# Kernel tuning notes

Hardware: AMD Instinct MI355X
Metric: run time of the kernel (lower is better)

The kernel has to match this reference:

```python
import jax, jax.numpy as jnp
import numpy as np

NEG_INF = -1.0e9


def setup_inputs() -> dict:
    key = jax.random.key(0)
    ks = jax.random.split(key, 8)
    B, H, S, D = 8, 8, 1024, 64
    return {
        "gv_feat": jax.random.normal(ks[0], (B, D), dtype=jnp.float32),
        "query2": jax.random.normal(ks[1], (B, H, S, D), dtype=jnp.float32),
        "key": jax.random.normal(ks[2], (B, H, S, D), dtype=jnp.float32),
        "att_mask": jax.random.randint(ks[3], (B, S), 0, 2, dtype=jnp.int32),
        "value1": jax.random.normal(ks[4], (B, H, S, D), dtype=jnp.float32),
        "value2": jax.random.normal(ks[5], (B, H, S, D), dtype=jnp.float32),
        "W_ch": jax.random.normal(ks[6], (D, D), dtype=jnp.float32) * (1.0 / np.sqrt(D)),
        "b_ch": jnp.zeros((D,), dtype=jnp.float32),
    }


def reference(gv_feat, query2, key, att_mask, value1, value2, W_ch, b_ch):
    # query2/key/value1/value2: [B, H, S, D]; att_mask: [B, S]
    D = query2.shape[-1]
    scaling = D ** (-0.5)
    # spatial attention: masked scaled QK^T softmax
    scores = jnp.einsum("bhqd,bhkd->bhqk", query2, key) * scaling  # [B,H,S,S]
    mask = att_mask[:, None, None, :]  # [B,1,1,S]
    scores = jnp.where(mask == 0, NEG_INF, scores)
    alpha_spatial = jax.nn.softmax(scores, axis=-1)
    attn2 = jnp.einsum("bhqk,bhkd->bhqd", alpha_spatial, value2)  # [B,H,S,D]
    # channel attention: sigmoid-gated linear over elementwise value1*key
    att_map_channel = value1 * key  # [B,H,S,D]
    alpha_channel = jax.nn.sigmoid(
        jnp.einsum("bhsd,ed->bhse", att_map_channel, W_ch) + b_ch
    )
    attn2 = alpha_channel * attn2
    return (gv_feat, attn2)
```

## Files before the change

### kernel.cpp

```cpp
#include <hip/hip_runtime.h>
#include <hip/hip_bf16.h>

typedef __attribute__((ext_vector_type(4)))  float f32x4;
typedef __attribute__((ext_vector_type(16))) float f32x16;
typedef __attribute__((ext_vector_type(8)))  short bf16x8;
typedef __attribute__((ext_vector_type(4)))  unsigned u32x4;
typedef __attribute__((ext_vector_type(2)))  unsigned u32x2;

#define NEG_INF_F (-1000000000.0f)

__device__ inline unsigned pkbf(float a, float b) {
    union { __hip_bfloat16 h; unsigned short u; } x, y;
    x.h = __float2bfloat16(a);
    y.h = __float2bfloat16(b);
    return (unsigned)x.u | ((unsigned)y.u << 16);
}

__global__ __launch_bounds__(1024) void aoa_prep_kernel(
    const int* __restrict__ maskp,
    int* __restrict__ vidx, float* __restrict__ padmask, int* __restrict__ nvalid)
{
    const int b   = blockIdx.x;
    const int tid = threadIdx.x;
    const int lane = tid & 63;

    const int m = maskp[b * 1024 + tid] ? 1 : 0;
    unsigned long long bal = __ballot(m);
    const int wpre = __popcll(bal & ((1ull << lane) - 1ull));

    __shared__ int wsum[16], woff[16];
    if (lane == 63) wsum[tid >> 6] = wpre + m;
    __syncthreads();
    if (tid < 16) {
        int off = 0;
        for (int i = 0; i < tid; ++i) off += wsum[i];
        woff[tid] = off;
    }
    __syncthreads();
    const int pos = woff[tid >> 6] + wpre;
    const int nv  = woff[15] + wsum[15];

    if (m) vidx[b * 1024 + pos] = tid;
    if (tid >= nv) vidx[b * 1024 + tid] = 0;
    padmask[b * 1024 + tid] = (tid < nv) ? 0.0f : NEG_INF_F;
    if (tid == 0) nvalid[b] = nv;
}

__global__ __launch_bounds__(512) void aoa_attn_kernel(
    const float* __restrict__ gv,
    const float* __restrict__ q2,
    const float* __restrict__ keyp,
    const float* __restrict__ v1,
    const float* __restrict__ v2,
    const float* __restrict__ W,
    const float* __restrict__ bch,
    const int*   __restrict__ vidx,
    const float* __restrict__ padmask,
    const int*   __restrict__ nvalid,
    float* __restrict__ out)
{
    constexpr int S = 1024, D = 64;
    const int bh  = blockIdx.x;
    const int qt  = blockIdx.y;
    const int b   = bh >> 3;
    const int tid = threadIdx.x;
    const int wid = tid >> 6;
    const int lane = tid & 63;
    const int l31 = lane & 31;
    const int h   = lane >> 5;

    float* out_attn = out + 512;
    if (bh == 0 && qt == 0) out[tid] = gv[tid];

    __shared__ float pmL[S];
    __shared__ int   vidxL[S];
    __shared__ short Klds[2][64][72];
    __shared__ short Vt[2][64][72];
    __shared__ float Lw[8][32];

    for (int i = tid; i < S; i += 512) {
        pmL[i]   = padmask[b * S + i];
        vidxL[i] = vidx[b * S + i];
    }

    const int nv = nvalid[b];
    const int NT = (nv + 63) >> 6;

    const size_t base = (size_t)bh * S * D;
    const float* Qp  = q2   + base;
    const float* Kp  = keyp + base;
    const float* V1p = v1   + base;
    const float* V2p = v2   + base;

    const int q0   = qt * 256 + wid * 32;
    const int qrow = q0 + l31;

    bf16x8 bq[4];
    #pragma unroll
    for (int ds = 0; ds < 4; ++ds) {
        const f32x4* p = (const f32x4*)(Qp + (size_t)qrow * D + ds * 16 + h * 8);
        f32x4 x0 = p[0], x1 = p[1];
        u32x4 u = (u32x4){pkbf(x0[0], x0[1]), pkbf(x0[2], x0[3]),
                          pkbf(x1[0], x1[1]), pkbf(x1[2], x1[3])};
        bq[ds] = *(bf16x8*)&u;
    }

    f32x16 acc_g[2];
    #pragma unroll
    for (int eh = 0; eh < 2; ++eh)
        #pragma unroll
        for (int r = 0; r < 16; ++r) acc_g[eh][r] = 0.0f;
    {
        bf16x8 bam[4];
        #pragma unroll
        for (int ds = 0; ds < 4; ++ds) {
            const f32x4* p1 = (const f32x4*)(V1p + (size_t)qrow * D + ds * 16 + h * 8);
            const f32x4* pk = (const f32x4*)(Kp  + (size_t)qrow * D + ds * 16 + h * 8);
            f32x4 a0 = p1[0], a1 = p1[1], c0 = pk[0], c1 = pk[1];
            u32x4 u = (u32x4){pkbf(a0[0]*c0[0], a0[1]*c0[1]), pkbf(a0[2]*c0[2], a0[3]*c0[3]),
                              pkbf(a1[0]*c1[0], a1[1]*c1[1]), pkbf(a1[2]*c1[2], a1[3]*c1[3])};
            bam[ds] = *(bf16x8*)&u;
        }
        #pragma unroll
        for (int eh = 0; eh < 2; ++eh) {
            #pragma unroll
            for (int ds = 0; ds < 4; ++ds) {
                const f32x4* pw = (const f32x4*)(W + (size_t)(eh * 32 + l31) * D + ds * 16 + h * 8);
                f32x4 x0 = pw[0], x1 = pw[1];
                u32x4 u = (u32x4){pkbf(x0[0], x0[1]), pkbf(x0[2], x0[3]),
                                  pkbf(x1[0], x1[1]), pkbf(x1[2], x1[3])};
                bf16x8 bw = *(bf16x8*)&u;
                acc_g[eh] = __builtin_amdgcn_mfma_f32_32x32x16_bf16(bam[ds], bw, acc_g[eh], 0, 0, 0);
            }
        }
    }

    f32x16 acc_o[2];
    #pragma unroll
    for (int dh = 0; dh < 2; ++dh)
        #pragma unroll
        for (int r = 0; r < 16; ++r) acc_o[dh][r] = 0.0f;

    float l_run = 0.0f;
    const float SC  = 0.125f * 1.4426950408889634f;
    const float SHF = 12.0f;

    const int kk   = tid >> 3;
    const int d0   = (tid & 7) << 3;
    const int dcol = tid & 63;
    const int kr0  = (tid >> 6) << 3;

    __syncthreads();

    f32x4 kA, kB;
    float vv[8];
    {
        const f32x4* src = (const f32x4*)(Kp + (size_t)vidxL[kk] * D + d0);
        kA = src[0]; kB = src[1];
        #pragma unroll
        for (int i = 0; i < 8; ++i) vv[i] = V2p[(size_t)vidxL[kr0 + i] * D + dcol];
    }
    *(u32x4*)&Klds[0][kk][d0] = (u32x4){pkbf(kA[0], kA[1]), pkbf(kA[2], kA[3]),
                                        pkbf(kB[0], kB[1]), pkbf(kB[2], kB[3])};
    *(u32x4*)&Vt[0][dcol][kr0] = (u32x4){pkbf(vv[0], vv[1]), pkbf(vv[2], vv[3]),
                                         pkbf(vv[4], vv[5]), pkbf(vv[6], vv[7])};
    int cur = 0;

    for (int t = 0; t < NT; ++t) {
        const int kt = t * 64;
        __syncthreads();

        if (t < NT - 1) {
            const f32x4* src = (const f32x4*)(Kp + (size_t)vidxL[kt + 64 + kk] * D + d0);
            kA = src[0]; kB = src[1];
            #pragma unroll
            for (int i = 0; i < 8; ++i) vv[i] = V2p[(size_t)vidxL[kt + 64 + kr0 + i] * D + dcol];
        }

        f32x16 a0;
        #pragma unroll
        for (int r = 0; r < 16; ++r) a0[r] = 0.0f;
        #pragma unroll
        for (int ds = 0; ds < 4; ++ds) {
            bf16x8 ak = *(const bf16x8*)&Klds[cur][l31][ds * 16 + h * 8];
            a0 = __builtin_amdgcn_mfma_f32_32x32x16_bf16(ak, bq[ds], a0, 0, 0, 0);
        }
        f32x16 a1;
        #pragma unroll
        for (int r = 0; r < 16; ++r) a1[r] = 0.0f;
        #pragma unroll
        for (int ds = 0; ds < 4; ++ds) {
            bf16x8 ak = *(const bf16x8*)&Klds[cur][32 + l31][ds * 16 + h * 8];
            a1 = __builtin_amdgcn_mfma_f32_32x32x16_bf16(ak, bq[ds], a1, 0, 0, 0);
        }

        unsigned w0[8];
        {
            float ps0 = 0.f, ps1 = 0.f;
            #pragma unroll
            for (int g = 0; g < 4; ++g) {
                f32x4 mk = *(const f32x4*)&pmL[kt + g * 8 + h * 4];
                float p0 = __builtin_amdgcn_exp2f(fmaf(a0[g * 4 + 0], SC, mk[0]) - SHF);
                float p1 = __builtin_amdgcn_exp2f(fmaf(a0[g * 4 + 1], SC, mk[1]) - SHF);
                float p2 = __builtin_amdgcn_exp2f(fmaf(a0[g * 4 + 2], SC, mk[2]) - SHF);
                float p3 = __builtin_amdgcn_exp2f(fmaf(a0[g * 4 + 3], SC, mk[3]) - SHF);
                ps0 += p0 + p1; ps1 += p2 + p3;
                w0[g * 2]     = pkbf(p0, p1);
                w0[g * 2 + 1] = pkbf(p2, p3);
            }
            float psum = ps0 + ps1;
            psum += __shfl_xor(psum, 32);
            l_run += psum;
        }

        #pragma unroll
        for (int t2 = 0; t2 < 2; ++t2) {
            u32x2 r0 = __builtin_amdgcn_permlane32_swap(w0[t2 * 4 + 0], w0[t2 * 4 + 2], false, false);
            u32x2 r1 = __builtin_amdgcn_permlane32_swap(w0[t2 * 4 + 1], w0[t2 * 4 + 3], false, false);
            u32x4 ua = (u32x4){r0[0], r1[0], r0[1], r1[1]};
            bf16x8 pa = *(bf16x8*)&ua;
            #pragma unroll
            for (int dh = 0; dh < 2; ++dh) {
                bf16x8 bv = *(const bf16x8*)&Vt[cur][dh * 32 + l31][t2 * 16 + h * 8];
                acc_o[dh] = __builtin_amdgcn_mfma_f32_32x32x16_bf16(pa, bv, acc_o[dh], 0, 0, 0);
            }
        }

        unsigned w1[8];
        {
            float ps0 = 0.f, ps1 = 0.f;
            #pragma unroll
            for (int g = 0; g < 4; ++g) {
                f32x4 mk = *(const f32x4*)&pmL[kt + 32 + g * 8 + h * 4];
                float p0 = __builtin_amdgcn_exp2f(fmaf(a1[g * 4 + 0], SC, mk[0]) - SHF);
                float p1 = __builtin_amdgcn_exp2f(fmaf(a1[g * 4 + 1], SC, mk[1]) - SHF);
                float p2 = __builtin_amdgcn_exp2f(fmaf(a1[g * 4 + 2], SC, mk[2]) - SHF);
                float p3 = __builtin_amdgcn_exp2f(fmaf(a1[g * 4 + 3], SC, mk[3]) - SHF);
                ps0 += p0 + p1; ps1 += p2 + p3;
                w1[g * 2]     = pkbf(p0, p1);
                w1[g * 2 + 1] = pkbf(p2, p3);
            }
            float psum = ps0 + ps1;
            psum += __shfl_xor(psum, 32);
            l_run += psum;
        }

        #pragma unroll
        for (int t2 = 0; t2 < 2; ++t2) {
            u32x2 r0 = __builtin_amdgcn_permlane32_swap(w1[t2 * 4 + 0], w1[t2 * 4 + 2], false, false);
            u32x2 r1 = __builtin_amdgcn_permlane32_swap(w1[t2 * 4 + 1], w1[t2 * 4 + 3], false, false);
            u32x4 ua = (u32x4){r0[0], r1[0], r0[1], r1[1]};
            bf16x8 pa = *(bf16x8*)&ua;
            #pragma unroll
            for (int dh = 0; dh < 2; ++dh) {
                bf16x8 bv = *(const bf16x8*)&Vt[cur][dh * 32 + l31][32 + t2 * 16 + h * 8];
                acc_o[dh] = __builtin_amdgcn_mfma_f32_32x32x16_bf16(pa, bv, acc_o[dh], 0, 0, 0);
            }
        }

        if (t < NT - 1) {
            *(u32x4*)&Klds[cur ^ 1][kk][d0] = (u32x4){pkbf(kA[0], kA[1]), pkbf(kA[2], kA[3]),
                                                      pkbf(kB[0], kB[1]), pkbf(kB[2], kB[3])};
            *(u32x4*)&Vt[cur ^ 1][dcol][kr0] = (u32x4){pkbf(vv[0], vv[1]), pkbf(vv[2], vv[3]),
                                                       pkbf(vv[4], vv[5]), pkbf(vv[6], vv[7])};
        }
        cur ^= 1;
    }

    Lw[wid][l31] = 1.0f / l_run;
    __builtin_amdgcn_wave_barrier();
    const float bv0 = bch[l31], bv1 = bch[32 + l31];
    #pragma unroll
    for (int dh = 0; dh < 2; ++dh) {
        const float bc = dh ? bv1 : bv0;
        #pragma unroll
        for (int r = 0; r < 16; ++r) {
            const int ql = (r & 3) + 8 * (r >> 2) + 4 * h;
            float invl = Lw[wid][ql];
            float o = acc_o[dh][r] * invl;
            float z = acc_g[dh][r] + bc;
            float gate = 1.0f / (1.0f + __expf(-z));
            out_attn[base + (size_t)(q0 + ql) * D + dh * 32 + l31] = o * gate;
        }
    }
}

extern "C" void kernel_launch(void* const* d_in, const int* in_sizes, int n_in,
                              void* d_out, int out_size, void* d_ws, size_t ws_size,
                              hipStream_t stream) {
    const float* gv   = (const float*)d_in[0];
    const float* q2   = (const float*)d_in[1];
    const float* keyp = (const float*)d_in[2];
    const int*   mask = (const int*)  d_in[3];
    const float* v1   = (const float*)d_in[4];
    const float* v2   = (const float*)d_in[5];
    const float* W    = (const float*)d_in[6];
    const float* bch  = (const float*)d_in[7];
    float* out = (float*)d_out;

    int*   vidx    = (int*)d_ws;
    float* padmask = (float*)(vidx + 8 * 1024);
    int*   nvalid  = (int*)(padmask + 8 * 1024);

    aoa_prep_kernel<<<8, 1024, 0, stream>>>(mask, vidx, padmask, nvalid);

    dim3 grid(64, 4);
    aoa_attn_kernel<<<grid, 512, 0, stream>>>(gv, q2, keyp, v1, v2, W, bch,
                                              vidx, padmask, nvalid, out);
}
```

Before: 41.24 us.

## Process two query sub-tiles per wave with 256-thread blocks and deferred gate GEMM

Each wave now handles 64 query rows (two 32-row sub-tiles) instead of 32, so every K/V fragment read from LDS feeds twice as many MFMAs. The block shrinks from 512 to 256 threads, and each thread gathers 16 elements per tile instead of 8. The channel-gate GEMM moves after the attention loop to keep register pressure down, and the row-sum reciprocal is broadcast with shuffles instead of going through LDS. The trade-off is twice the accumulator registers per wave and half as many waves per block to hide latency.

```diff
diff --git a/kernel.cpp b/kernel.cpp
--- a/kernel.cpp
+++ b/kernel.cpp
@@ -46,7 +46,7 @@
     if (tid == 0) nvalid[b] = nv;
 }
 
-__global__ __launch_bounds__(512) void aoa_attn_kernel(
+__global__ __launch_bounds__(256, 1) void aoa_attn_kernel(
     const float* __restrict__ gv,
     const float* __restrict__ q2,
     const float* __restrict__ keyp,
@@ -70,15 +70,14 @@
     const int h   = lane >> 5;
 
     float* out_attn = out + 512;
-    if (bh == 0 && qt == 0) out[tid] = gv[tid];
+    if (bh == 0 && qt == 0) { out[tid] = gv[tid]; out[tid + 256] = gv[tid + 256]; }
 
     __shared__ float pmL[S];
     __shared__ int   vidxL[S];
     __shared__ short Klds[2][64][72];
     __shared__ short Vt[2][64][72];
-    __shared__ float Lw[8][32];
-
-    for (int i = tid; i < S; i += 512) {
+
+    for (int i = tid; i < S; i += 256) {
         pmL[i]   = padmask[b * S + i];
         vidxL[i] = vidx[b * S + i];
     }
@@ -92,78 +91,58 @@
     const float* V1p = v1   + base;
     const float* V2p = v2   + base;
 
-    const int q0   = qt * 256 + wid * 32;
-    const int qrow = q0 + l31;
-
-    bf16x8 bq[4];
+    const int q0  = qt * 256 + wid * 64;
+    const int qa  = q0 + l31;
+    const int qb  = q0 + 32 + l31;
+
+    bf16x8 bqa[4], bqb[4];
     #pragma unroll
     for (int ds = 0; ds < 4; ++ds) {
-        const f32x4* p = (const f32x4*)(Qp + (size_t)qrow * D + ds * 16 + h * 8);
-        f32x4 x0 = p[0], x1 = p[1];
-        u32x4 u = (u32x4){pkbf(x0[0], x0[1]), pkbf(x0[2], x0[3]),
-                          pkbf(x1[0], x1[1]), pkbf(x1[2], x1[3])};
-        bq[ds] = *(bf16x8*)&u;
-    }
-
-    f32x16 acc_g[2];
-    #pragma unroll
-    for (int eh = 0; eh < 2; ++eh)
-        #pragma unroll
-        for (int r = 0; r < 16; ++r) acc_g[eh][r] = 0.0f;
-    {
-        bf16x8 bam[4];
-        #pragma unroll
-        for (int ds = 0; ds < 4; ++ds) {
-            const f32x4* p1 = (const f32x4*)(V1p + (size_t)qrow * D + ds * 16 + h * 8);
-            const f32x4* pk = (const f32x4*)(Kp  + (size_t)qrow * D + ds * 16 + h * 8);
-            f32x4 a0 = p1[0], a1 = p1[1], c0 = pk[0], c1 = pk[1];
-            u32x4 u = (u32x4){pkbf(a0[0]*c0[0], a0[1]*c0[1]), pkbf(a0[2]*c0[2], a0[3]*c0[3]),
-                              pkbf(a1[0]*c1[0], a1[1]*c1[1]), pkbf(a1[2]*c1[2], a1[3]*c1[3])};
-            bam[ds] = *(bf16x8*)&u;
-        }
-        #pragma unroll
-        for (int eh = 0; eh < 2; ++eh) {
-            #pragma unroll
-            for (int ds = 0; ds < 4; ++ds) {
-                const f32x4* pw = (const f32x4*)(W + (size_t)(eh * 32 + l31) * D + ds * 16 + h * 8);
-                f32x4 x0 = pw[0], x1 = pw[1];
-                u32x4 u = (u32x4){pkbf(x0[0], x0[1]), pkbf(x0[2], x0[3]),
-                                  pkbf(x1[0], x1[1]), pkbf(x1[2], x1[3])};
-                bf16x8 bw = *(bf16x8*)&u;
-                acc_g[eh] = __builtin_amdgcn_mfma_f32_32x32x16_bf16(bam[ds], bw, acc_g[eh], 0, 0, 0);
-            }
-        }
-    }
-
-    f32x16 acc_o[2];
+        const f32x4* pa = (const f32x4*)(Qp + (size_t)qa * D + ds * 16 + h * 8);
+        f32x4 x0 = pa[0], x1 = pa[1];
+        u32x4 ua = (u32x4){pkbf(x0[0], x0[1]), pkbf(x0[2], x0[3]),
+                           pkbf(x1[0], x1[1]), pkbf(x1[2], x1[3])};
+        bqa[ds] = *(bf16x8*)&ua;
+        const f32x4* pb = (const f32x4*)(Qp + (size_t)qb * D + ds * 16 + h * 8);
+        f32x4 y0 = pb[0], y1 = pb[1];
+        u32x4 ub = (u32x4){pkbf(y0[0], y0[1]), pkbf(y0[2], y0[3]),
+                           pkbf(y1[0], y1[1]), pkbf(y1[2], y1[3])};
+        bqb[ds] = *(bf16x8*)&ub;
+    }
+
+    f32x16 acc_oa[2], acc_ob[2];
     #pragma unroll
     for (int dh = 0; dh < 2; ++dh)
         #pragma unroll
-        for (int r = 0; r < 16; ++r) acc_o[dh][r] = 0.0f;
-
-    float l_run = 0.0f;
+        for (int r = 0; r < 16; ++r) { acc_oa[dh][r] = 0.0f; acc_ob[dh][r] = 0.0f; }
+
+    float l_a = 0.0f, l_b = 0.0f;
     const float SC  = 0.125f * 1.4426950408889634f;
     const float SHF = 12.0f;
 
-    const int kk   = tid >> 3;
-    const int d0   = (tid & 7) << 3;
+    const int kk   = tid >> 2;
+    const int d0   = (tid & 3) << 4;
     const int dcol = tid & 63;
-    const int kr0  = (tid >> 6) << 3;
+    const int kr0  = (tid >> 6) << 4;
 
     __syncthreads();
 
-    f32x4 kA, kB;
-    float vv[8];
+    f32x4 kA0, kA1, kA2, kA3;
+    float vv[16];
     {
         const f32x4* src = (const f32x4*)(Kp + (size_t)vidxL[kk] * D + d0);
-        kA = src[0]; kB = src[1];
-        #pragma unroll
-        for (int i = 0; i < 8; ++i) vv[i] = V2p[(size_t)vidxL[kr0 + i] * D + dcol];
-    }
-    *(u32x4*)&Klds[0][kk][d0] = (u32x4){pkbf(kA[0], kA[1]), pkbf(kA[2], kA[3]),
-                                        pkbf(kB[0], kB[1]), pkbf(kB[2], kB[3])};
-    *(u32x4*)&Vt[0][dcol][kr0] = (u32x4){pkbf(vv[0], vv[1]), pkbf(vv[2], vv[3]),
-                                         pkbf(vv[4], vv[5]), pkbf(vv[6], vv[7])};
+        kA0 = src[0]; kA1 = src[1]; kA2 = src[2]; kA3 = src[3];
+        #pragma unroll
+        for (int i = 0; i < 16; ++i) vv[i] = V2p[(size_t)vidxL[kr0 + i] * D + dcol];
+    }
+    *(u32x4*)&Klds[0][kk][d0]     = (u32x4){pkbf(kA0[0], kA0[1]), pkbf(kA0[2], kA0[3]),
+                                            pkbf(kA1[0], kA1[1]), pkbf(kA1[2], kA1[3])};
+    *(u32x4*)&Klds[0][kk][d0 + 8] = (u32x4){pkbf(kA2[0], kA2[1]), pkbf(kA2[2], kA2[3]),
+                                            pkbf(kA3[0], kA3[1]), pkbf(kA3[2], kA3[3])};
+    *(u32x4*)&Vt[0][dcol][kr0]     = (u32x4){pkbf(vv[0], vv[1]),  pkbf(vv[2], vv[3]),
+                                             pkbf(vv[4], vv[5]),  pkbf(vv[6], vv[7])};
+    *(u32x4*)&Vt[0][dcol][kr0 + 8] = (u32x4){pkbf(vv[8], vv[9]),  pkbf(vv[10], vv[11]),
+                                             pkbf(vv[12], vv[13]), pkbf(vv[14], vv[15])};
     int cur = 0;
 
     for (int t = 0; t < NT; ++t) {
@@ -172,103 +151,192 @@
 
         if (t < NT - 1) {
             const f32x4* src = (const f32x4*)(Kp + (size_t)vidxL[kt + 64 + kk] * D + d0);
-            kA = src[0]; kB = src[1];
-            #pragma unroll
-            for (int i = 0; i < 8; ++i) vv[i] = V2p[(size_t)vidxL[kt + 64 + kr0 + i] * D + dcol];
-        }
-
-        f32x16 a0;
-        #pragma unroll
-        for (int r = 0; r < 16; ++r) a0[r] = 0.0f;
+            kA0 = src[0]; kA1 = src[1]; kA2 = src[2]; kA3 = src[3];
+            #pragma unroll
+            for (int i = 0; i < 16; ++i) vv[i] = V2p[(size_t)vidxL[kt + 64 + kr0 + i] * D + dcol];
+        }
+
+        f32x16 a0a, a1a, a0b, a1b;
+        #pragma unroll
+        for (int r = 0; r < 16; ++r) { a0a[r] = 0.f; a1a[r] = 0.f; a0b[r] = 0.f; a1b[r] = 0.f; }
         #pragma unroll
         for (int ds = 0; ds < 4; ++ds) {
             bf16x8 ak = *(const bf16x8*)&Klds[cur][l31][ds * 16 + h * 8];
-            a0 = __builtin_amdgcn_mfma_f32_32x32x16_bf16(ak, bq[ds], a0, 0, 0, 0);
-        }
-        f32x16 a1;
-        #pragma unroll
-        for (int r = 0; r < 16; ++r) a1[r] = 0.0f;
+            a0a = __builtin_amdgcn_mfma_f32_32x32x16_bf16(ak, bqa[ds], a0a, 0, 0, 0);
+            a0b = __builtin_amdgcn_mfma_f32_32x32x16_bf16(ak, bqb[ds], a0b, 0, 0, 0);
+        }
         #pragma unroll
         for (int ds = 0; ds < 4; ++ds) {
             bf16x8 ak = *(const bf16x8*)&Klds[cur][32 + l31][ds * 16 + h * 8];
-            a1 = __builtin_amdgcn_mfma_f32_32x32x16_bf16(ak, bq[ds], a1, 0, 0, 0);
-        }
-
-        unsigned w0[8];
+            a1a = __builtin_amdgcn_mfma_f32_32x32x16_bf16(ak, bqa[ds], a1a, 0, 0, 0);
+            a1b = __builtin_amdgcn_mfma_f32_32x32x16_bf16(ak, bqb[ds], a1b, 0, 0, 0);
+        }
+
+        unsigned w0a[8], w1a[8], w0b[8], w1b[8];
         {
             float ps0 = 0.f, ps1 = 0.f;
             #pragma unroll
             for (int g = 0; g < 4; ++g) {
                 f32x4 mk = *(const f32x4*)&pmL[kt + g * 8 + h * 4];
-                float p0 = __builtin_amdgcn_exp2f(fmaf(a0[g * 4 + 0], SC, mk[0]) - SHF);
-                float p1 = __builtin_amdgcn_exp2f(fmaf(a0[g * 4 + 1], SC, mk[1]) - SHF);
-                float p2 = __builtin_amdgcn_exp2f(fmaf(a0[g * 4 + 2], SC, mk[2]) - SHF);
-                float p3 = __builtin_amdgcn_exp2f(fmaf(a0[g * 4 + 3], SC, mk[3]) - SHF);
+                float p0 = __builtin_amdgcn_exp2f(fmaf(a0a[g * 4 + 0], SC, mk[0]) - SHF);
+                float p1 = __builtin_amdgcn_exp2f(fmaf(a0a[g * 4 + 1], SC, mk[1]) - SHF);
+                float p2 = __builtin_amdgcn_exp2f(fmaf(a0a[g * 4 + 2], SC, mk[2]) - SHF);
+                float p3 = __builtin_amdgcn_exp2f(fmaf(a0a[g * 4 + 3], SC, mk[3]) - SHF);
                 ps0 += p0 + p1; ps1 += p2 + p3;
-                w0[g * 2]     = pkbf(p0, p1);
-                w0[g * 2 + 1] = pkbf(p2, p3);
+                w0a[g * 2] = pkbf(p0, p1); w0a[g * 2 + 1] = pkbf(p2, p3);
             }
             float psum = ps0 + ps1;
             psum += __shfl_xor(psum, 32);
-            l_run += psum;
-        }
-
+            l_a += psum;
+        }
         #pragma unroll
         for (int t2 = 0; t2 < 2; ++t2) {
-            u32x2 r0 = __builtin_amdgcn_permlane32_swap(w0[t2 * 4 + 0], w0[t2 * 4 + 2], false, false);
-            u32x2 r1 = __builtin_amdgcn_permlane32_swap(w0[t2 * 4 + 1], w0[t2 * 4 + 3], false, false);
+            u32x2 r0 = __builtin_amdgcn_permlane32_swap(w0a[t2 * 4 + 0], w0a[t2 * 4 + 2], false, false);
+            u32x2 r1 = __builtin_amdgcn_permlane32_swap(w0a[t2 * 4 + 1], w0a[t2 * 4 + 3], false, false);
             u32x4 ua = (u32x4){r0[0], r1[0], r0[1], r1[1]};
             bf16x8 pa = *(bf16x8*)&ua;
             #pragma unroll
             for (int dh = 0; dh < 2; ++dh) {
                 bf16x8 bv = *(const bf16x8*)&Vt[cur][dh * 32 + l31][t2 * 16 + h * 8];
-                acc_o[dh] = __builtin_amdgcn_mfma_f32_32x32x16_bf16(pa, bv, acc_o[dh], 0, 0, 0);
-            }
-        }
-
-        unsigned w1[8];
+                acc_oa[dh] = __builtin_amdgcn_mfma_f32_32x32x16_bf16(pa, bv, acc_oa[dh], 0, 0, 0);
+            }
+        }
         {
             float ps0 = 0.f, ps1 = 0.f;
             #pragma unroll
             for (int g = 0; g < 4; ++g) {
-                f32x4 mk = *(const f32x4*)&pmL[kt + 32 + g * 8 + h * 4];
-                float p0 = __builtin_amdgcn_exp2f(fmaf(a1[g * 4 + 0], SC, mk[0]) - SHF);
-                float p1 = __builtin_amdgcn_exp2f(fmaf(a1[g * 4 + 1], SC, mk[1]) - SHF);
-                float p2 = __builtin_amdgcn_exp2f(fmaf(a1[g * 4 + 2], SC, mk[2]) - SHF);
-                float p3 = __builtin_amdgcn_exp2f(fmaf(a1[g * 4 + 3], SC, mk[3]) - SHF);
+                f32x4 mk = *(const f32x4*)&pmL[kt + g * 8 + h * 4];
+                float p0 = __builtin_amdgcn_exp2f(fmaf(a0b[g * 4 + 0], SC, mk[0]) - SHF);
+                float p1 = __builtin_amdgcn_exp2f(fmaf(a0b[g * 4 + 1], SC, mk[1]) - SHF);
+                float p2 = __builtin_amdgcn_exp2f(fmaf(a0b[g * 4 + 2], SC, mk[2]) - SHF);
+                float p3 = __builtin_amdgcn_exp2f(fmaf(a0b[g * 4 + 3], SC, mk[3]) - SHF);
                 ps0 += p0 + p1; ps1 += p2 + p3;
-                w1[g * 2]     = pkbf(p0, p1);
-                w1[g * 2 + 1] = pkbf(p2, p3);
+                w0b[g * 2] = pkbf(p0, p1); w0b[g * 2 + 1] = pkbf(p2, p3);
             }
             float psum = ps0 + ps1;
             psum += __shfl_xor(psum, 32);
-            l_run += psum;
-        }
-
+            l_b += psum;
+        }
         #pragma unroll
         for (int t2 = 0; t2 < 2; ++t2) {
-            u32x2 r0 = __builtin_amdgcn_permlane32_swap(w1[t2 * 4 + 0], w1[t2 * 4 + 2], false, false);
-            u32x2 r1 = __builtin_amdgcn_permlane32_swap(w1[t2 * 4 + 1], w1[t2 * 4 + 3], false, false);
+            u32x2 r0 = __builtin_amdgcn_permlane32_swap(w0b[t2 * 4 + 0], w0b[t2 * 4 + 2], false, false);
+            u32x2 r1 = __builtin_amdgcn_permlane32_swap(w0b[t2 * 4 + 1], w0b[t2 * 4 + 3], false, false);
             u32x4 ua = (u32x4){r0[0], r1[0], r0[1], r1[1]};
             bf16x8 pa = *(bf16x8*)&ua;
             #pragma unroll
             for (int dh = 0; dh < 2; ++dh) {
+                bf16x8 bv = *(const bf16x8*)&Vt[cur][dh * 32 + l31][t2 * 16 + h * 8];
+                acc_ob[dh] = __builtin_amdgcn_mfma_f32_32x32x16_bf16(pa, bv, acc_ob[dh], 0, 0, 0);
+            }
+        }
+        {
+            float ps0 = 0.f, ps1 = 0.f;
+            #pragma unroll
+            for (int g = 0; g < 4; ++g) {
+                f32x4 mk = *(const f32x4*)&pmL[kt + 32 + g * 8 + h * 4];
+                float p0 = __builtin_amdgcn_exp2f(fmaf(a1a[g * 4 + 0], SC, mk[0]) - SHF);
+                float p1 = __builtin_amdgcn_exp2f(fmaf(a1a[g * 4 + 1], SC, mk[1]) - SHF);
+                float p2 = __builtin_amdgcn_exp2f(fmaf(a1a[g * 4 + 2], SC, mk[2]) - SHF);
+                float p3 = __builtin_amdgcn_exp2f(fmaf(a1a[g * 4 + 3], SC, mk[3]) - SHF);
+                ps0 += p0 + p1; ps1 += p2 + p3;
+                w1a[g * 2] = pkbf(p0, p1); w1a[g * 2 + 1] = pkbf(p2, p3);
+            }
+            float psum = ps0 + ps1;
+            psum += __shfl_xor(psum, 32);
+            l_a += psum;
+        }
+        #pragma unroll
+        for (int t2 = 0; t2 < 2; ++t2) {
+            u32x2 r0 = __builtin_amdgcn_permlane32_swap(w1a[t2 * 4 + 0], w1a[t2 * 4 + 2], false, false);
+            u32x2 r1 = __builtin_amdgcn_permlane32_swap(w1a[t2 * 4 + 1], w1a[t2 * 4 + 3], false, false);
+            u32x4 ua = (u32x4){r0[0], r1[0], r0[1], r1[1]};
+            bf16x8 pa = *(bf16x8*)&ua;
+            #pragma unroll
+            for (int dh = 0; dh < 2; ++dh) {
                 bf16x8 bv = *(const bf16x8*)&Vt[cur][dh * 32 + l31][32 + t2 * 16 + h * 8];
-                acc_o[dh] = __builtin_amdgcn_mfma_f32_32x32x16_bf16(pa, bv, acc_o[dh], 0, 0, 0);
+                acc_oa[dh] = __builtin_amdgcn_mfma_f32_32x32x16_bf16(pa, bv, acc_oa[dh], 0, 0, 0);
+            }
+        }
+        {
+            float ps0 = 0.f, ps1 = 0.f;
+            #pragma unroll
+            for (int g = 0; g < 4; ++g) {
+                f32x4 mk = *(const f32x4*)&pmL[kt + 32 + g * 8 + h * 4];
+                float p0 = __builtin_amdgcn_exp2f(fmaf(a1b[g * 4 + 0], SC, mk[0]) - SHF);
+                float p1 = __builtin_amdgcn_exp2f(fmaf(a1b[g * 4 + 1], SC, mk[1]) - SHF);
+                float p2 = __builtin_amdgcn_exp2f(fmaf(a1b[g * 4 + 2], SC, mk[2]) - SHF);
+                float p3 = __builtin_amdgcn_exp2f(fmaf(a1b[g * 4 + 3], SC, mk[3]) - SHF);
+                ps0 += p0 + p1; ps1 += p2 + p3;
+                w1b[g * 2] = pkbf(p0, p1); w1b[g * 2 + 1] = pkbf(p2, p3);
+            }
+            float psum = ps0 + ps1;
+            psum += __shfl_xor(psum, 32);
+            l_b += psum;
+        }
+        #pragma unroll
+        for (int t2 = 0; t2 < 2; ++t2) {
+            u32x2 r0 = __builtin_amdgcn_permlane32_swap(w1b[t2 * 4 + 0], w1b[t2 * 4 + 2], false, false);
+            u32x2 r1 = __builtin_amdgcn_permlane32_swap(w1b[t2 * 4 + 1], w1b[t2 * 4 + 3], false, false);
+            u32x4 ua = (u32x4){r0[0], r1[0], r0[1], r1[1]};
+            bf16x8 pa = *(bf16x8*)&ua;
+            #pragma unroll
+            for (int dh = 0; dh < 2; ++dh) {
+                bf16x8 bv = *(const bf16x8*)&Vt[cur][dh * 32 + l31][32 + t2 * 16 + h * 8];
+                acc_ob[dh] = __builtin_amdgcn_mfma_f32_32x32x16_bf16(pa, bv, acc_ob[dh], 0, 0, 0);
             }
         }
 
         if (t < NT - 1) {
-            *(u32x4*)&Klds[cur ^ 1][kk][d0] = (u32x4){pkbf(kA[0], kA[1]), pkbf(kA[2], kA[3]),
-                                                      pkbf(kB[0], kB[1]), pkbf(kB[2], kB[3])};
-            *(u32x4*)&Vt[cur ^ 1][dcol][kr0] = (u32x4){pkbf(vv[0], vv[1]), pkbf(vv[2], vv[3]),
-                                                       pkbf(vv[4], vv[5]), pkbf(vv[6], vv[7])};
+            *(u32x4*)&Klds[cur ^ 1][kk][d0]     = (u32x4){pkbf(kA0[0], kA0[1]), pkbf(kA0[2], kA0[3]),
+                                                          pkbf(kA1[0], kA1[1]), pkbf(kA1[2], kA1[3])};
+            *(u32x4*)&Klds[cur ^ 1][kk][d0 + 8] = (u32x4){pkbf(kA2[0], kA2[1]), pkbf(kA2[2], kA2[3]),
+                                                          pkbf(kA3[0], kA3[1]), pkbf(kA3[2], kA3[3])};
+            *(u32x4*)&Vt[cur ^ 1][dcol][kr0]     = (u32x4){pkbf(vv[0], vv[1]),  pkbf(vv[2], vv[3]),
+                                                           pkbf(vv[4], vv[5]),  pkbf(vv[6], vv[7])};
+            *(u32x4*)&Vt[cur ^ 1][dcol][kr0 + 8] = (u32x4){pkbf(vv[8], vv[9]),  pkbf(vv[10], vv[11]),
+                                                           pkbf(vv[12], vv[13]), pkbf(vv[14], vv[15])};
         }
         cur ^= 1;
     }
 
-    Lw[wid][l31] = 1.0f / l_run;
-    __builtin_amdgcn_wave_barrier();
+    f32x16 acc_ga[2], acc_gb[2];
+    #pragma unroll
+    for (int eh = 0; eh < 2; ++eh)
+        #pragma unroll
+        for (int r = 0; r < 16; ++r) { acc_ga[eh][r] = 0.0f; acc_gb[eh][r] = 0.0f; }
+
+    bf16x8 bama[4], bamb[4];
+    #pragma unroll
+    for (int ds = 0; ds < 4; ++ds) {
+        const f32x4* p1a = (const f32x4*)(V1p + (size_t)qa * D + ds * 16 + h * 8);
+        const f32x4* pka = (const f32x4*)(Kp  + (size_t)qa * D + ds * 16 + h * 8);
+        f32x4 a0 = p1a[0], a1 = p1a[1], c0 = pka[0], c1 = pka[1];
+        u32x4 ua = (u32x4){pkbf(a0[0]*c0[0], a0[1]*c0[1]), pkbf(a0[2]*c0[2], a0[3]*c0[3]),
+                           pkbf(a1[0]*c1[0], a1[1]*c1[1]), pkbf(a1[2]*c1[2], a1[3]*c1[3])};
+        bama[ds] = *(bf16x8*)&ua;
+        const f32x4* p1b = (const f32x4*)(V1p + (size_t)qb * D + ds * 16 + h * 8);
+        const f32x4* pkb = (const f32x4*)(Kp  + (size_t)qb * D + ds * 16 + h * 8);
+        f32x4 b0 = p1b[0], b1 = p1b[1], d0v = pkb[0], d1v = pkb[1];
+        u32x4 ub = (u32x4){pkbf(b0[0]*d0v[0], b0[1]*d0v[1]), pkbf(b0[2]*d0v[2], b0[3]*d0v[3]),
+                           pkbf(b1[0]*d1v[0], b1[1]*d1v[1]), pkbf(b1[2]*d1v[2], b1[3]*d1v[3])};
+        bamb[ds] = *(bf16x8*)&ub;
+    }
+    #pragma unroll
+    for (int eh = 0; eh < 2; ++eh) {
+        #pragma unroll
+        for (int ds = 0; ds < 4; ++ds) {
+            const f32x4* pw = (const f32x4*)(W + (size_t)(eh * 32 + l31) * D + ds * 16 + h * 8);
+            f32x4 x0 = pw[0], x1 = pw[1];
+            u32x4 u = (u32x4){pkbf(x0[0], x0[1]), pkbf(x0[2], x0[3]),
+                              pkbf(x1[0], x1[1]), pkbf(x1[2], x1[3])};
+            bf16x8 bw = *(bf16x8*)&u;
+            acc_ga[eh] = __builtin_amdgcn_mfma_f32_32x32x16_bf16(bama[ds], bw, acc_ga[eh], 0, 0, 0);
+            acc_gb[eh] = __builtin_amdgcn_mfma_f32_32x32x16_bf16(bamb[ds], bw, acc_gb[eh], 0, 0, 0);
+        }
+    }
+
+    const float inv_a = 1.0f / l_a;
+    const float inv_b = 1.0f / l_b;
     const float bv0 = bch[l31], bv1 = bch[32 + l31];
     #pragma unroll
     for (int dh = 0; dh < 2; ++dh) {
@@ -276,11 +344,17 @@
         #pragma unroll
         for (int r = 0; r < 16; ++r) {
             const int ql = (r & 3) + 8 * (r >> 2) + 4 * h;
-            float invl = Lw[wid][ql];
-            float o = acc_o[dh][r] * invl;
-            float z = acc_g[dh][r] + bc;
-            float gate = 1.0f / (1.0f + __expf(-z));
-            out_attn[base + (size_t)(q0 + ql) * D + dh * 32 + l31] = o * gate;
+            float ia = __shfl(inv_a, ql);
+            float oa = acc_oa[dh][r] * ia;
+            float za = acc_ga[dh][r] + bc;
+            float ga = 1.0f / (1.0f + __expf(-za));
+            out_attn[base + (size_t)(q0 + ql) * D + dh * 32 + l31] = oa * ga;
+
+            float ib = __shfl(inv_b, ql);
+            float ob = acc_ob[dh][r] * ib;
+            float zb = acc_gb[dh][r] + bc;
+            float gb = 1.0f / (1.0f + __expf(-zb));
+            out_attn[base + (size_t)(q0 + 32 + ql) * D + dh * 32 + l31] = ob * gb;
         }
     }
 }
@@ -305,6 +379,6 @@
     aoa_prep_kernel<<<8, 1024, 0, stream>>>(mask, vidx, padmask, nvalid);
 
     dim3 grid(64, 4);
-    aoa_attn_kernel<<<grid, 512, 0, stream>>>(gv, q2, keyp, v1, v2, W, bch,
+    aoa_attn_kernel<<<grid, 256, 0, stream>>>(gv, q2, keyp, v1, v2, W, bch,
                                               vidx, padmask, nvalid, out);
 }
```

After: 45.80 us. +11.1%, slower.
